# Kernel tuning notes

Hardware: AMD Instinct MI355X
Metric: run time of the kernel (lower is better)

The kernel has to match this reference:

```python
import jax, jax.numpy as jnp
import numpy as np

B = 256
D = 512
C = 100000
S = 30.0
M = 0.5
COS_M = float(np.cos(M))
SIN_M = float(np.sin(M))
TH = float(np.cos(np.pi - M))
MM = float(np.sin(np.pi - M) * M)


def setup_inputs() -> dict:
    key = jax.random.key(0)
    k1, k2, k3, k4 = jax.random.split(key, 4)
    image_emb = jax.random.normal(k1, (B, D), dtype=jnp.float32)
    profile_emb = jax.random.normal(k2, (B, D), dtype=jnp.float32)
    # xavier_uniform_ for weight [C, D]: bound = sqrt(6/(C+D))
    bound = float(np.sqrt(6.0 / (C + D)))
    weight = jax.random.uniform(k3, (C, D), dtype=jnp.float32, minval=-bound, maxval=bound)
    label = jax.random.randint(k4, (B,), 0, C, dtype=jnp.int64)
    return {"image_emb": image_emb, "profile_emb": profile_emb, "weight": weight, "label": label}


def reference(image_emb, profile_emb, weight, label):
    emb = jnp.concatenate([image_emb, profile_emb], axis=0)          # [2B, D]
    lab = jnp.tile(label, (2,))                                      # [2B]
    emb_n = emb / jnp.linalg.norm(emb, axis=1, keepdims=True)
    w_n = weight / jnp.linalg.norm(weight, axis=1, keepdims=True)
    cosine = jnp.einsum('nd,cd->nc', emb_n, w_n)                     # [2B, C]
    sine = jnp.sqrt(jnp.clip(1.0 - cosine * cosine, 0.0, 1.0))
    phi = cosine * COS_M - sine * SIN_M
    phi = jnp.where(cosine > TH, phi, cosine - MM)                   # easy_margin=False
    one_hot = jnp.arange(cosine.shape[1])[None, :] == lab[:, None]   # [2B, C] bool
    logits = S * jnp.where(one_hot, phi, cosine)
    logp = jax.nn.log_softmax(logits, axis=1)
    nll = -jnp.take_along_axis(logp, lab[:, None], axis=1)[:, 0]
    return jnp.mean(nll)
```

## Files before the change

kernel.cpp:

```cpp
#include <hip/hip_runtime.h>

#define S_SCALE 30.0f
#define COS_M 0.8775825618903728f
#define SIN_M 0.479425538604203f
#define TH_C (-0.8775825618903728f)
#define MM_C 0.2397127693021015f

#define BD 512
#define DD 512
#define CC 100000
#define NCB 1563
#define LASTB 1562

typedef __bf16 bf16x8 __attribute__((ext_vector_type(8)));
typedef __bf16 bf16x4 __attribute__((ext_vector_type(4)));
typedef float  f32x4  __attribute__((ext_vector_type(4)));

__global__ __launch_bounds__(256) void k_prep(const float* __restrict__ img,
                                              const float* __restrict__ prof,
                                              const float* __restrict__ W,
                                              const int* __restrict__ lab,
                                              __bf16* __restrict__ At,
                                              float* __restrict__ sphi,
                                              float* __restrict__ scos) {
    const int t = threadIdx.x;
    const int wave = t >> 6, l = t & 63;
    const int row = blockIdx.x * 4 + wave;
    const float* src = (row < 256) ? (img + (size_t)row * DD) : (prof + (size_t)(row - 256) * DD);
    float4 v0 = ((const float4*)src)[l * 2];
    float4 v1 = ((const float4*)src)[l * 2 + 1];
    float s = v0.x * v0.x + v0.y * v0.y + v0.z * v0.z + v0.w * v0.w
            + v1.x * v1.x + v1.y * v1.y + v1.z * v1.z + v1.w * v1.w;
    #pragma unroll
    for (int o = 1; o < 64; o <<= 1) s += __shfl_xor(s, o);
    float r = rsqrtf(s);
    bf16x8 a;
    a[0] = (__bf16)(v0.x * r); a[1] = (__bf16)(v0.y * r);
    a[2] = (__bf16)(v0.z * r); a[3] = (__bf16)(v0.w * r);
    a[4] = (__bf16)(v1.x * r); a[5] = (__bf16)(v1.y * r);
    a[6] = (__bf16)(v1.z * r); a[7] = (__bf16)(v1.w * r);
    *(bf16x8*)(At + (size_t)(l >> 2) * (BD * 32) + row * 32 + (l & 3) * 8) = a;

    const int c = lab[row & 255];
    const float4* wc = (const float4*)(W + (size_t)c * DD);
    float4 w0 = wc[l * 2], w1 = wc[l * 2 + 1];
    float wb0 = (float)(__bf16)w0.x, wb1 = (float)(__bf16)w0.y;
    float wb2 = (float)(__bf16)w0.z, wb3 = (float)(__bf16)w0.w;
    float wb4 = (float)(__bf16)w1.x, wb5 = (float)(__bf16)w1.y;
    float wb6 = (float)(__bf16)w1.z, wb7 = (float)(__bf16)w1.w;
    float dot = (float)a[0] * wb0 + (float)a[1] * wb1 + (float)a[2] * wb2 + (float)a[3] * wb3
              + (float)a[4] * wb4 + (float)a[5] * wb5 + (float)a[6] * wb6 + (float)a[7] * wb7;
    float wsq = wb0 * wb0 + wb1 * wb1 + wb2 * wb2 + wb3 * wb3
              + wb4 * wb4 + wb5 * wb5 + wb6 * wb6 + wb7 * wb7;
    #pragma unroll
    for (int o = 1; o < 64; o <<= 1) { dot += __shfl_xor(dot, o); wsq += __shfl_xor(wsq, o); }
    if (l == 0) {
        float cs = dot * rsqrtf(wsq);
        float sn = sqrtf(fmaxf(0.f, fminf(1.f, 1.f - cs * cs)));
        float phi = cs * COS_M - sn * SIN_M;
        if (!(cs > TH_C)) phi = cs - MM_C;
        sphi[row] = S_SCALE * phi;
        scos[row] = S_SCALE * cs;
    }
}

__global__ __launch_bounds__(256, 2) void k_gemm(const __bf16* __restrict__ At,
                                                 const float* __restrict__ W,
                                                 float* __restrict__ part) {
    __shared__ __bf16 Bs[2][64 * 32];
    __shared__ float  csq[64];

    const int t = threadIdx.x;
    const int cb = blockIdx.x;
    const int wave = t >> 6, lane = t & 63, q = lane >> 4, m16 = lane & 15;

    const int frag_off = m16 * 32 + ((q ^ ((m16 >> 1) & 3)) << 3);

    const int wcol = t >> 3, kc = t & 7;
    int gc0 = cb * 64 + wcol;
    int gc1 = gc0 + 32;
    const float* wp0 = W + (size_t)(gc0 < CC ? gc0 : 0) * DD + kc * 4;
    const float* wp1 = W + (size_t)(gc1 < CC ? gc1 : 0) * DD + kc * 4;
    const int sxw   = (kc >> 1) ^ ((wcol >> 1) & 3);
    const int wofs0 = wcol * 32 + sxw * 8 + (kc & 1) * 4;
    const int wofs1 = wofs0 + 1024;

    const __bf16* ap = At + (size_t)(wave * 128 + m16) * 32 + q * 8;

    f32x4 acc[8][4] = {};
    float sq0 = 0.f, sq1 = 0.f;
    bf16x8 a[2][8];
    float4 wv0[16], wv1[16];

#define CVT_BS(buf, va, vb)                                                             \
    {                                                                                   \
        bf16x4 b0 = { (__bf16)(va).x, (__bf16)(va).y, (__bf16)(va).z, (__bf16)(va).w }; \
        bf16x4 b1 = { (__bf16)(vb).x, (__bf16)(vb).y, (__bf16)(vb).z, (__bf16)(vb).w }; \
        float f;                                                                        \
        f = (float)b0[0]; sq0 += f * f; f = (float)b0[1]; sq0 += f * f;                 \
        f = (float)b0[2]; sq0 += f * f; f = (float)b0[3]; sq0 += f * f;                 \
        f = (float)b1[0]; sq1 += f * f; f = (float)b1[1]; sq1 += f * f;                 \
        f = (float)b1[2]; sq1 += f * f; f = (float)b1[3]; sq1 += f * f;                 \
        *(bf16x4*)(&Bs[buf][wofs0]) = b0;                                               \
        *(bf16x4*)(&Bs[buf][wofs1]) = b1;                                               \
    }

    #pragma unroll
    for (int i = 0; i < 8; ++i)
        a[0][i] = *(const bf16x8*)(ap + i * 512);
    wv0[0] = *(const float4*)(wp0);        wv1[0] = *(const float4*)(wp1);
    wv0[1] = *(const float4*)(wp0 + 32);   wv1[1] = *(const float4*)(wp1 + 32);
    wv0[2] = *(const float4*)(wp0 + 64);   wv1[2] = *(const float4*)(wp1 + 64);
    CVT_BS(0, wv0[0], wv1[0]);

    #pragma unroll
    for (int kt = 0; kt < 16; ++kt) {
        if (kt < 15) {
            #pragma unroll
            for (int i = 0; i < 8; ++i)
                a[(kt + 1) & 1][i] = *(const bf16x8*)(ap + (kt + 1) * 16384 + i * 512);
        }
        if (kt + 3 < 16) {
            wv0[kt + 3] = *(const float4*)(wp0 + (kt + 3) * 32);
            wv1[kt + 3] = *(const float4*)(wp1 + (kt + 3) * 32);
        }
        __builtin_amdgcn_sched_barrier(0);
        asm volatile("s_waitcnt lgkmcnt(0)");
        __builtin_amdgcn_s_barrier();
        __builtin_amdgcn_sched_barrier(0);

        bf16x8 bfrag[4];
        #pragma unroll
        for (int j = 0; j < 4; ++j)
            bfrag[j] = *(const bf16x8*)(&Bs[kt & 1][j * 512 + frag_off]);

        if (kt < 15) CVT_BS((kt + 1) & 1, wv0[kt + 1], wv1[kt + 1]);

        __builtin_amdgcn_s_setprio(1);
        #pragma unroll
        for (int i = 0; i < 8; ++i) {
            #pragma unroll
            for (int j = 0; j < 4; ++j)
                acc[i][j] = __builtin_amdgcn_mfma_f32_16x16x32_bf16(a[kt & 1][i], bfrag[j],
                                                                    acc[i][j], 0, 0, 0);
        }
        __builtin_amdgcn_s_setprio(0);
    }

    sq0 += __shfl_xor(sq0, 1); sq1 += __shfl_xor(sq1, 1);
    sq0 += __shfl_xor(sq0, 2); sq1 += __shfl_xor(sq1, 2);
    sq0 += __shfl_xor(sq0, 4); sq1 += __shfl_xor(sq1, 4);
    if (kc == 0) { csq[wcol] = sq0; csq[wcol + 32] = sq1; }
    __syncthreads();

    const bool lastb = (cb == LASTB);
    float inv[4]; bool val[4];
    #pragma unroll
    for (int j = 0; j < 4; ++j) {
        int ct = j * 16 + m16;
        val[j] = (!lastb) || (ct < 32);
        inv[j] = rsqrtf(csq[ct]) * S_SCALE;
    }
    #pragma unroll
    for (int i = 0; i < 8; ++i) {
        #pragma unroll
        for (int r = 0; r < 4; ++r) {
            float e = 0.f;
            #pragma unroll
            for (int j = 0; j < 4; ++j)
                if (val[j]) e += __expf(acc[i][j][r] * inv[j]);
            e += __shfl_xor(e, 1);
            e += __shfl_xor(e, 2);
            e += __shfl_xor(e, 4);
            e += __shfl_xor(e, 8);
            if (m16 == 0)
                part[(size_t)cb * BD + wave * 128 + i * 16 + q * 4 + r] = e;
        }
    }
#undef CVT_BS
}

__global__ __launch_bounds__(256) void k_reduce1(const float* __restrict__ part,
                                                 float* __restrict__ rowpart) {
    const int b = blockIdx.x;
    const int rg = b >> 5, cp = b & 31;
    const int t = threadIdx.x;
    const int rl = t & 63, ph = t >> 6;
    const int r0 = rg * 64;
    float s = 0.f;
    for (int c0 = cp * 4 + ph; c0 < NCB; c0 += 128)
        s += part[(size_t)c0 * BD + r0 + rl];
    __shared__ float buf[256];
    buf[t] = s;
    __syncthreads();
    if (t < 64)
        rowpart[(size_t)cp * BD + r0 + t] = buf[t] + buf[t + 64] + buf[t + 128] + buf[t + 192];
}

__global__ __launch_bounds__(256) void k_final(const float* __restrict__ rowpart,
                                               const float* __restrict__ sphi,
                                               const float* __restrict__ scos,
                                               float* __restrict__ out) {
    const int t = threadIdx.x;
    float a = 0.f;
    for (int r = t; r < BD; r += 256) {
        float total = 0.f;
        #pragma unroll
        for (int cp = 0; cp < 32; ++cp)
            total += rowpart[(size_t)cp * BD + r];
        float lse = logf(total);
        float sp = sphi[r], sc = scos[r];
        float corr = log1pf(__expf(sp - lse) - __expf(sc - lse));
        a += lse + corr - sp;
    }
    for (int o = 1; o < 64; o <<= 1) a += __shfl_xor(a, o);
    __shared__ float wsum[4];
    if ((t & 63) == 0) wsum[t >> 6] = a;
    __syncthreads();
    if (t == 0) out[0] = (wsum[0] + wsum[1] + wsum[2] + wsum[3]) * (1.0f / 512.0f);
}

extern "C" void kernel_launch(void* const* d_in, const int* in_sizes, int n_in,
                              void* d_out, int out_size, void* d_ws, size_t ws_size,
                              hipStream_t stream) {
    const float* img  = (const float*)d_in[0];
    const float* prof = (const float*)d_in[1];
    const float* W    = (const float*)d_in[2];
    const int*   lab  = (const int*)d_in[3];

    char* ws = (char*)d_ws;
    __bf16* At     = (__bf16*)ws;
    float* sphi    = (float*)(ws + 524288);
    float* scos    = (float*)(ws + 526336);
    float* part    = (float*)(ws + 528384);
    float* rowpart = (float*)(ws + 3729408);

    k_prep<<<128, 256, 0, stream>>>(img, prof, W, lab, At, sphi, scos);
    k_gemm<<<NCB, 256, 0, stream>>>(At, W, part);
    k_reduce1<<<256, 256, 0, stream>>>(part, rowpart);
    k_final<<<1, 256, 0, stream>>>(rowpart, sphi, scos, (float*)d_out);
}
```

Before: 325.9 us.

## Ring-buffer A fragments and interleave next-tile loads with split MFMA halves

Replaces the double-buffered 16-entry A fragment array with a 12-slot ring. The next tile's A loads are split into two halves, each issued around one half of the MFMA block, so fewer vector registers stay live. The W prefetch becomes a 4-deep rotating buffer, up from 3-ahead. The bf16 conversion and LDS store of the next W tile now happen after the MFMAs. The aim is to lower register pressure and overlap global loads with matrix math. The risk is exposing load latency inside the MFMA sequence and delaying the LDS write before the next barrier.

```diff
diff --git a/kernel.cpp b/kernel.cpp
--- a/kernel.cpp
+++ b/kernel.cpp
@@ -89,8 +89,8 @@
 
     f32x4 acc[8][4] = {};
     float sq0 = 0.f, sq1 = 0.f;
-    bf16x8 a[2][8];
-    float4 wv0[16], wv1[16];
+    bf16x8 ar[12];
+    float4 wva[4], wvb[4];
 
 #define CVT_BS(buf, va, vb)                                                             \
     {                                                                                   \
@@ -106,24 +106,28 @@
     }
 
     #pragma unroll
-    for (int i = 0; i < 8; ++i)
-        a[0][i] = *(const bf16x8*)(ap + i * 512);
-    wv0[0] = *(const float4*)(wp0);        wv1[0] = *(const float4*)(wp1);
-    wv0[1] = *(const float4*)(wp0 + 32);   wv1[1] = *(const float4*)(wp1 + 32);
-    wv0[2] = *(const float4*)(wp0 + 64);   wv1[2] = *(const float4*)(wp1 + 64);
-    CVT_BS(0, wv0[0], wv1[0]);
+    for (int f = 0; f < 8; ++f)
+        ar[f] = *(const bf16x8*)(ap + f * 512);
+    #pragma unroll
+    for (int n = 0; n < 4; ++n) {
+        wva[n] = *(const float4*)(wp0 + n * 32);
+        wvb[n] = *(const float4*)(wp1 + n * 32);
+    }
+    CVT_BS(0, wva[0], wvb[0]);
 
     #pragma unroll
     for (int kt = 0; kt < 16; ++kt) {
+        if (kt + 4 < 16) {
+            wva[(kt + 4) & 3] = *(const float4*)(wp0 + (kt + 4) * 32);
+            wvb[(kt + 4) & 3] = *(const float4*)(wp1 + (kt + 4) * 32);
+        }
         if (kt < 15) {
             #pragma unroll
-            for (int i = 0; i < 8; ++i)
-                a[(kt + 1) & 1][i] = *(const bf16x8*)(ap + (kt + 1) * 16384 + i * 512);
-        }
-        if (kt + 3 < 16) {
-            wv0[kt + 3] = *(const float4*)(wp0 + (kt + 3) * 32);
-            wv1[kt + 3] = *(const float4*)(wp1 + (kt + 3) * 32);
-        }
+            for (int f = 0; f < 4; ++f)
+                ar[((kt + 1) * 8 + f) % 12] =
+                    *(const bf16x8*)(ap + (kt + 1) * 16384 + f * 512);
+        }
+
         __builtin_amdgcn_sched_barrier(0);
         asm volatile("s_waitcnt lgkmcnt(0)");
         __builtin_amdgcn_s_barrier();
@@ -134,17 +138,35 @@
         for (int j = 0; j < 4; ++j)
             bfrag[j] = *(const bf16x8*)(&Bs[kt & 1][j * 512 + frag_off]);
 
-        if (kt < 15) CVT_BS((kt + 1) & 1, wv0[kt + 1], wv1[kt + 1]);
-
         __builtin_amdgcn_s_setprio(1);
         #pragma unroll
-        for (int i = 0; i < 8; ++i) {
+        for (int i = 0; i < 4; ++i) {
             #pragma unroll
             for (int j = 0; j < 4; ++j)
-                acc[i][j] = __builtin_amdgcn_mfma_f32_16x16x32_bf16(a[kt & 1][i], bfrag[j],
-                                                                    acc[i][j], 0, 0, 0);
+                acc[i][j] = __builtin_amdgcn_mfma_f32_16x16x32_bf16(
+                    ar[(kt * 8 + i) % 12], bfrag[j], acc[i][j], 0, 0, 0);
         }
         __builtin_amdgcn_s_setprio(0);
+
+        if (kt < 15) {
+            #pragma unroll
+            for (int f = 4; f < 8; ++f)
+                ar[((kt + 1) * 8 + f) % 12] =
+                    *(const bf16x8*)(ap + (kt + 1) * 16384 + f * 512);
+        }
+
+        __builtin_amdgcn_s_setprio(1);
+        #pragma unroll
+        for (int i = 4; i < 8; ++i) {
+            #pragma unroll
+            for (int j = 0; j < 4; ++j)
+                acc[i][j] = __builtin_amdgcn_mfma_f32_16x16x32_bf16(
+                    ar[(kt * 8 + i) % 12], bfrag[j], acc[i][j], 0, 0, 0);
+        }
+        __builtin_amdgcn_s_setprio(0);
+
+        __builtin_amdgcn_sched_barrier(0);
+        if (kt < 15) CVT_BS((kt + 1) & 1, wva[(kt + 1) & 3], wvb[(kt + 1) & 3]);
     }
 
     sq0 += __shfl_xor(sq0, 1); sq1 += __shfl_xor(sq1, 1);
```

New measurement: 325.6 us. No clear change (-0.1%).

## Widen GEMM tile to 128 classes and stage activations via direct global-to-LDS loads

Applied to the files above, without the earlier changes.

Each GEMM block now uses 512 threads and covers 128 weight columns instead of 64, arranged as 2 column groups by 4 row groups of waves. The bf16 activation tile is streamed into shared memory with global_load_lds across a 4-deep ring, so waves share it instead of each loading A fragments into registers. Weight loads are pipelined four tiles ahead with hand-tuned vmcnt waits, and the partial-sum layout and reduction bounds are updated to match. This aims to halve redundant activation traffic per class and free registers. In exchange it uses much more LDS (about 144KB per block), which may limit occupancy, and the hand-counted waits are fragile.

```diff
diff --git a/kernel.cpp b/kernel.cpp
--- a/kernel.cpp
+++ b/kernel.cpp
@@ -9,12 +9,15 @@
 #define BD 512
 #define DD 512
 #define CC 100000
-#define NCB 1563
-#define LASTB 1562
+#define NCB2 782
+#define LASTB2 781
+#define NPART 1564
 
 typedef __bf16 bf16x8 __attribute__((ext_vector_type(8)));
-typedef __bf16 bf16x4 __attribute__((ext_vector_type(4)));
 typedef float  f32x4  __attribute__((ext_vector_type(4)));
+
+#define AS1 __attribute__((address_space(1)))
+#define AS3 __attribute__((address_space(3)))
 
 __global__ __launch_bounds__(256) void k_prep(const float* __restrict__ img,
                                               const float* __restrict__ prof,
@@ -64,100 +67,120 @@
     }
 }
 
-__global__ __launch_bounds__(256, 2) void k_gemm(const __bf16* __restrict__ At,
+__global__ __launch_bounds__(512, 2) void k_gemm(const __bf16* __restrict__ At,
                                                  const float* __restrict__ W,
                                                  float* __restrict__ part) {
-    __shared__ __bf16 Bs[2][64 * 32];
-    __shared__ float  csq[64];
+    __shared__ __bf16 As[4][BD * 32];
+    __shared__ __bf16 Bs[2][128 * 32];
+    __shared__ float  csq[128];
 
     const int t = threadIdx.x;
     const int cb = blockIdx.x;
     const int wave = t >> 6, lane = t & 63, q = lane >> 4, m16 = lane & 15;
+    const int rg = wave >> 1;
+    const int cg = wave & 1;
 
     const int frag_off = m16 * 32 + ((q ^ ((m16 >> 1) & 3)) << 3);
 
-    const int wcol = t >> 3, kc = t & 7;
-    int gc0 = cb * 64 + wcol;
-    int gc1 = gc0 + 32;
-    const float* wp0 = W + (size_t)(gc0 < CC ? gc0 : 0) * DD + kc * 4;
-    const float* wp1 = W + (size_t)(gc1 < CC ? gc1 : 0) * DD + kc * 4;
-    const int sxw   = (kc >> 1) ^ ((wcol >> 1) & 3);
-    const int wofs0 = wcol * 32 + sxw * 8 + (kc & 1) * 4;
-    const int wofs1 = wofs0 + 1024;
-
-    const __bf16* ap = At + (size_t)(wave * 128 + m16) * 32 + q * 8;
+    const int wcol = t >> 2, kc = t & 3;
+    const int gc = cb * 128 + wcol;
+    const float* wp = W + (size_t)(gc < CC ? gc : 0) * DD + kc * 8;
+    const int wofs = wcol * 32 + ((kc ^ ((wcol >> 1) & 3)) << 3);
+
+    const int srcswz = ((t >> 2) << 6) + ((((t & 3) ^ ((t >> 3) & 3))) << 4);
 
     f32x4 acc[8][4] = {};
-    float sq0 = 0.f, sq1 = 0.f;
-    bf16x8 a[2][8];
-    float4 wv0[16], wv1[16];
+    float sq = 0.f;
+    float4 wva[4], wvb[4];
+
+#define GLDS_TILE(kt, buf)                                                              \
+    {                                                                                   \
+        const char* gsrc = (const char*)At + (size_t)(kt) * 32768 + srcswz;             \
+        _Pragma("unroll")                                                               \
+        for (int c4 = 0; c4 < 4; ++c4) {                                                \
+            __builtin_amdgcn_global_load_lds(                                           \
+                (AS1 void*)(gsrc + c4 * 8192),                                          \
+                (AS3 void*)((char*)(&As[buf][0]) + c4 * 8192 + wave * 1024),            \
+                16, 0, 0);                                                              \
+        }                                                                               \
+    }
+
+#define LOAD_W(n)                                                                       \
+    {                                                                                   \
+        wva[(n) & 3] = *(const float4*)(wp + (n) * 32);                                 \
+        wvb[(n) & 3] = *(const float4*)(wp + (n) * 32 + 4);                             \
+    }
 
 #define CVT_BS(buf, va, vb)                                                             \
     {                                                                                   \
-        bf16x4 b0 = { (__bf16)(va).x, (__bf16)(va).y, (__bf16)(va).z, (__bf16)(va).w }; \
-        bf16x4 b1 = { (__bf16)(vb).x, (__bf16)(vb).y, (__bf16)(vb).z, (__bf16)(vb).w }; \
+        bf16x8 b;                                                                       \
+        b[0] = (__bf16)(va).x; b[1] = (__bf16)(va).y;                                   \
+        b[2] = (__bf16)(va).z; b[3] = (__bf16)(va).w;                                   \
+        b[4] = (__bf16)(vb).x; b[5] = (__bf16)(vb).y;                                   \
+        b[6] = (__bf16)(vb).z; b[7] = (__bf16)(vb).w;                                   \
         float f;                                                                        \
-        f = (float)b0[0]; sq0 += f * f; f = (float)b0[1]; sq0 += f * f;                 \
-        f = (float)b0[2]; sq0 += f * f; f = (float)b0[3]; sq0 += f * f;                 \
-        f = (float)b1[0]; sq1 += f * f; f = (float)b1[1]; sq1 += f * f;                 \
-        f = (float)b1[2]; sq1 += f * f; f = (float)b1[3]; sq1 += f * f;                 \
-        *(bf16x4*)(&Bs[buf][wofs0]) = b0;                                               \
-        *(bf16x4*)(&Bs[buf][wofs1]) = b1;                                               \
-    }
-
-    #pragma unroll
-    for (int i = 0; i < 8; ++i)
-        a[0][i] = *(const bf16x8*)(ap + i * 512);
-    wv0[0] = *(const float4*)(wp0);        wv1[0] = *(const float4*)(wp1);
-    wv0[1] = *(const float4*)(wp0 + 32);   wv1[1] = *(const float4*)(wp1 + 32);
-    wv0[2] = *(const float4*)(wp0 + 64);   wv1[2] = *(const float4*)(wp1 + 64);
-    CVT_BS(0, wv0[0], wv1[0]);
-
-    #pragma unroll
-    for (int kt = 0; kt < 16; ++kt) {
-        if (kt < 15) {
-            #pragma unroll
-            for (int i = 0; i < 8; ++i)
-                a[(kt + 1) & 1][i] = *(const bf16x8*)(ap + (kt + 1) * 16384 + i * 512);
-        }
-        if (kt + 3 < 16) {
-            wv0[kt + 3] = *(const float4*)(wp0 + (kt + 3) * 32);
-            wv1[kt + 3] = *(const float4*)(wp1 + (kt + 3) * 32);
-        }
-        __builtin_amdgcn_sched_barrier(0);
-        asm volatile("s_waitcnt lgkmcnt(0)");
-        __builtin_amdgcn_s_barrier();
-        __builtin_amdgcn_sched_barrier(0);
-
-        bf16x8 bfrag[4];
-        #pragma unroll
-        for (int j = 0; j < 4; ++j)
-            bfrag[j] = *(const bf16x8*)(&Bs[kt & 1][j * 512 + frag_off]);
-
-        if (kt < 15) CVT_BS((kt + 1) & 1, wv0[kt + 1], wv1[kt + 1]);
-
-        __builtin_amdgcn_s_setprio(1);
-        #pragma unroll
-        for (int i = 0; i < 8; ++i) {
-            #pragma unroll
-            for (int j = 0; j < 4; ++j)
-                acc[i][j] = __builtin_amdgcn_mfma_f32_16x16x32_bf16(a[kt & 1][i], bfrag[j],
-                                                                    acc[i][j], 0, 0, 0);
-        }
-        __builtin_amdgcn_s_setprio(0);
-    }
-
-    sq0 += __shfl_xor(sq0, 1); sq1 += __shfl_xor(sq1, 1);
-    sq0 += __shfl_xor(sq0, 2); sq1 += __shfl_xor(sq1, 2);
-    sq0 += __shfl_xor(sq0, 4); sq1 += __shfl_xor(sq1, 4);
-    if (kc == 0) { csq[wcol] = sq0; csq[wcol + 32] = sq1; }
+        f = (float)b[0]; sq += f * f; f = (float)b[1]; sq += f * f;                     \
+        f = (float)b[2]; sq += f * f; f = (float)b[3]; sq += f * f;                     \
+        f = (float)b[4]; sq += f * f; f = (float)b[5]; sq += f * f;                     \
+        f = (float)b[6]; sq += f * f; f = (float)b[7]; sq += f * f;                     \
+        *(bf16x8*)(&Bs[buf][wofs]) = b;                                                 \
+    }
+
+#define SB() __builtin_amdgcn_sched_barrier(0)
+
+#define ITER(kt, VM)                                                                    \
+    {                                                                                   \
+        if ((kt) + 2 <= 15) GLDS_TILE((kt) + 2, ((kt) + 2) & 3);                        \
+        SB();                                                                           \
+        if ((kt) + 4 <= 15) LOAD_W((kt) + 4);                                           \
+        SB();                                                                           \
+        asm volatile("s_waitcnt vmcnt(" #VM ") lgkmcnt(0)" ::: "memory");               \
+        __builtin_amdgcn_s_barrier();                                                   \
+        SB();                                                                           \
+        bf16x8 bfrag[4];                                                                \
+        _Pragma("unroll")                                                               \
+        for (int j = 0; j < 4; ++j)                                                     \
+            bfrag[j] = *(const bf16x8*)(&Bs[(kt) & 1][cg * 2048 + j * 512 + frag_off]); \
+        __builtin_amdgcn_s_setprio(1);                                                  \
+        _Pragma("unroll")                                                               \
+        for (int i = 0; i < 8; ++i) {                                                   \
+            bf16x8 afrag =                                                              \
+                *(const bf16x8*)(&As[(kt) & 3][rg * 4096 + i * 512 + frag_off]);        \
+            _Pragma("unroll")                                                           \
+            for (int j = 0; j < 4; ++j)                                                 \
+                acc[i][j] = __builtin_amdgcn_mfma_f32_16x16x32_bf16(                    \
+                    afrag, bfrag[j], acc[i][j], 0, 0, 0);                               \
+        }                                                                               \
+        __builtin_amdgcn_s_setprio(0);                                                  \
+        SB();                                                                           \
+        if ((kt) + 1 <= 15) CVT_BS(((kt) + 1) & 1, wva[((kt) + 1) & 3],                 \
+                                   wvb[((kt) + 1) & 3]);                                \
+    }
+
+    LOAD_W(0); LOAD_W(1);
+    SB();
+    GLDS_TILE(0, 0); GLDS_TILE(1, 1);
+    SB();
+    LOAD_W(2); LOAD_W(3);
+    SB();
+    CVT_BS(0, wva[0], wvb[0]);
+
+    ITER(0, 14);  ITER(1, 16);
+    ITER(2, 14);  ITER(3, 14);  ITER(4, 14);  ITER(5, 14);
+    ITER(6, 14);  ITER(7, 14);  ITER(8, 14);  ITER(9, 14);
+    ITER(10, 14); ITER(11, 14);
+    ITER(12, 12); ITER(13, 10); ITER(14, 4);  ITER(15, 0);
+
+    sq += __shfl_xor(sq, 1);
+    sq += __shfl_xor(sq, 2);
+    if (kc == 0) csq[wcol] = sq;
     __syncthreads();
 
-    const bool lastb = (cb == LASTB);
+    const bool lastb = (cb == LASTB2);
     float inv[4]; bool val[4];
     #pragma unroll
     for (int j = 0; j < 4; ++j) {
-        int ct = j * 16 + m16;
+        int ct = cg * 64 + j * 16 + m16;
         val[j] = (!lastb) || (ct < 32);
         inv[j] = rsqrtf(csq[ct]) * S_SCALE;
     }
@@ -174,10 +197,14 @@
             e += __shfl_xor(e, 4);
             e += __shfl_xor(e, 8);
             if (m16 == 0)
-                part[(size_t)cb * BD + wave * 128 + i * 16 + q * 4 + r] = e;
+                part[((size_t)cb * 2 + cg) * BD + rg * 128 + i * 16 + q * 4 + r] = e;
         }
     }
+#undef GLDS_TILE
+#undef LOAD_W
 #undef CVT_BS
+#undef SB
+#undef ITER
 }
 
 __global__ __launch_bounds__(256) void k_reduce1(const float* __restrict__ part,
@@ -188,7 +215,7 @@
     const int rl = t & 63, ph = t >> 6;
     const int r0 = rg * 64;
     float s = 0.f;
-    for (int c0 = cp * 4 + ph; c0 < NCB; c0 += 128)
+    for (int c0 = cp * 4 + ph; c0 < NPART; c0 += 128)
         s += part[(size_t)c0 * BD + r0 + rl];
     __shared__ float buf[256];
     buf[t] = s;
@@ -233,10 +260,10 @@
     float* sphi    = (float*)(ws + 524288);
     float* scos    = (float*)(ws + 526336);
     float* part    = (float*)(ws + 528384);
-    float* rowpart = (float*)(ws + 3729408);
+    float* rowpart = (float*)(ws + 3731456);
 
     k_prep<<<128, 256, 0, stream>>>(img, prof, W, lab, At, sphi, scos);
-    k_gemm<<<NCB, 256, 0, stream>>>(At, W, part);
+    k_gemm<<<NCB2, 512, 0, stream>>>(At, W, part);
     k_reduce1<<<256, 256, 0, stream>>>(part, rowpart);
     k_final<<<1, 256, 0, stream>>>(rowpart, sphi, scos, (float*)d_out);
 }
```

Result: slower. 344.9 us (+5.8%).

## Retile GEMM to 128x128 blocks with LDS-staged A via global_load_lds

Applied to the files above, without the earlier changes.

The GEMM is restructured from 64-class blocks holding all 512 rows in registers to 128-row by 128-class tiles with a 2x2 wave layout. A tiles are streamed into LDS via direct global-to-LDS loads instead of per-wave register loads. A block-index swizzle groups the four row blocks of a class tile, and occupancy is raised to 3 blocks per CU through a smaller accumulator footprint. Each W tile is now read and converted four times, once per row block, which raises W traffic unless L2 absorbs the repeats. The last block's validity mask (ct < 32) may be wrong for wc=1 under the new 128-class tiling.

```diff
diff --git a/kernel.cpp b/kernel.cpp
--- a/kernel.cpp
+++ b/kernel.cpp
@@ -9,12 +9,15 @@
 #define BD 512
 #define DD 512
 #define CC 100000
-#define NCB 1563
-#define LASTB 1562
+#define NCB2 782
+#define LASTB2 781
+#define NPART 1564
 
 typedef __bf16 bf16x8 __attribute__((ext_vector_type(8)));
-typedef __bf16 bf16x4 __attribute__((ext_vector_type(4)));
 typedef float  f32x4  __attribute__((ext_vector_type(4)));
+
+#define AS1 __attribute__((address_space(1)))
+#define AS3 __attribute__((address_space(3)))
 
 __global__ __launch_bounds__(256) void k_prep(const float* __restrict__ img,
                                               const float* __restrict__ prof,
@@ -64,105 +67,130 @@
     }
 }
 
-__global__ __launch_bounds__(256, 2) void k_gemm(const __bf16* __restrict__ At,
+__global__ __launch_bounds__(256, 3) void k_gemm(const __bf16* __restrict__ At,
                                                  const float* __restrict__ W,
                                                  float* __restrict__ part) {
-    __shared__ __bf16 Bs[2][64 * 32];
-    __shared__ float  csq[64];
-
-    const int t = threadIdx.x;
-    const int cb = blockIdx.x;
+    __shared__ __bf16 As[2][128 * 32];
+    __shared__ __bf16 Bs[2][128 * 32];
+
+    const int t = threadIdx.x;
+    const int bid = blockIdx.x;
+    const int swz = (bid & 7) * 391 + (bid >> 3);
+    const int rb = swz & 3;
+    const int cb = swz >> 2;
     const int wave = t >> 6, lane = t & 63, q = lane >> 4, m16 = lane & 15;
+    const int wr = wave >> 1, wc = wave & 1;
 
     const int frag_off = m16 * 32 + ((q ^ ((m16 >> 1) & 3)) << 3);
 
-    const int wcol = t >> 3, kc = t & 7;
-    int gc0 = cb * 64 + wcol;
-    int gc1 = gc0 + 32;
-    const float* wp0 = W + (size_t)(gc0 < CC ? gc0 : 0) * DD + kc * 4;
-    const float* wp1 = W + (size_t)(gc1 < CC ? gc1 : 0) * DD + kc * 4;
-    const int sxw   = (kc >> 1) ^ ((wcol >> 1) & 3);
-    const int wofs0 = wcol * 32 + sxw * 8 + (kc & 1) * 4;
-    const int wofs1 = wofs0 + 1024;
-
-    const __bf16* ap = At + (size_t)(wave * 128 + m16) * 32 + q * 8;
-
-    f32x4 acc[8][4] = {};
-    float sq0 = 0.f, sq1 = 0.f;
-    bf16x8 a[2][8];
-    float4 wv0[16], wv1[16];
-
-#define CVT_BS(buf, va, vb)                                                             \
-    {                                                                                   \
-        bf16x4 b0 = { (__bf16)(va).x, (__bf16)(va).y, (__bf16)(va).z, (__bf16)(va).w }; \
-        bf16x4 b1 = { (__bf16)(vb).x, (__bf16)(vb).y, (__bf16)(vb).z, (__bf16)(vb).w }; \
+    const int wcol = t >> 1, h = t & 1;
+    const int gc = cb * 128 + wcol;
+    const float* wp = W + (size_t)(gc < CC ? gc : 0) * DD + h * 16;
+    const int bofs0 = wcol * 32 + (((h * 2 + 0) ^ ((wcol >> 1) & 3)) << 3);
+    const int bofs1 = wcol * 32 + (((h * 2 + 1) ^ ((wcol >> 1) & 3)) << 3);
+
+    const int srcswz = ((t >> 2) << 6) + ((((t & 3) ^ ((t >> 3) & 3))) << 4);
+    const char* abase = (const char*)At + (size_t)rb * 8192 + srcswz;
+
+    f32x4 acc[4][4] = {};
+    float sq = 0.f;
+    float4 wr0, wr1, wr2, wr3;
+    bf16x8 nb0, nb1;
+
+#define GLDS_TILE(kt, buf)                                                              \
+    {                                                                                   \
+        _Pragma("unroll")                                                               \
+        for (int rr = 0; rr < 2; ++rr) {                                                \
+            __builtin_amdgcn_global_load_lds(                                           \
+                (AS1 void*)(abase + (size_t)(kt) * 32768 + rr * 4096),                  \
+                (AS3 void*)((char*)(&As[buf][0]) + rr * 4096 + wave * 1024),            \
+                16, 0, 0);                                                              \
+        }                                                                               \
+    }
+
+#define LOADW(n)                                                                        \
+    {                                                                                   \
+        wr0 = *(const float4*)(wp + (n) * 32);                                          \
+        wr1 = *(const float4*)(wp + (n) * 32 + 4);                                      \
+        wr2 = *(const float4*)(wp + (n) * 32 + 8);                                      \
+        wr3 = *(const float4*)(wp + (n) * 32 + 12);                                     \
+    }
+
+#define CVTW()                                                                          \
+    {                                                                                   \
+        nb0[0] = (__bf16)wr0.x; nb0[1] = (__bf16)wr0.y;                                 \
+        nb0[2] = (__bf16)wr0.z; nb0[3] = (__bf16)wr0.w;                                 \
+        nb0[4] = (__bf16)wr1.x; nb0[5] = (__bf16)wr1.y;                                 \
+        nb0[6] = (__bf16)wr1.z; nb0[7] = (__bf16)wr1.w;                                 \
+        nb1[0] = (__bf16)wr2.x; nb1[1] = (__bf16)wr2.y;                                 \
+        nb1[2] = (__bf16)wr2.z; nb1[3] = (__bf16)wr2.w;                                 \
+        nb1[4] = (__bf16)wr3.x; nb1[5] = (__bf16)wr3.y;                                 \
+        nb1[6] = (__bf16)wr3.z; nb1[7] = (__bf16)wr3.w;                                 \
         float f;                                                                        \
-        f = (float)b0[0]; sq0 += f * f; f = (float)b0[1]; sq0 += f * f;                 \
-        f = (float)b0[2]; sq0 += f * f; f = (float)b0[3]; sq0 += f * f;                 \
-        f = (float)b1[0]; sq1 += f * f; f = (float)b1[1]; sq1 += f * f;                 \
-        f = (float)b1[2]; sq1 += f * f; f = (float)b1[3]; sq1 += f * f;                 \
-        *(bf16x4*)(&Bs[buf][wofs0]) = b0;                                               \
-        *(bf16x4*)(&Bs[buf][wofs1]) = b1;                                               \
-    }
-
-    #pragma unroll
-    for (int i = 0; i < 8; ++i)
-        a[0][i] = *(const bf16x8*)(ap + i * 512);
-    wv0[0] = *(const float4*)(wp0);        wv1[0] = *(const float4*)(wp1);
-    wv0[1] = *(const float4*)(wp0 + 32);   wv1[1] = *(const float4*)(wp1 + 32);
-    wv0[2] = *(const float4*)(wp0 + 64);   wv1[2] = *(const float4*)(wp1 + 64);
-    CVT_BS(0, wv0[0], wv1[0]);
+        f = (float)nb0[0]; sq += f * f; f = (float)nb0[1]; sq += f * f;                 \
+        f = (float)nb0[2]; sq += f * f; f = (float)nb0[3]; sq += f * f;                 \
+        f = (float)nb0[4]; sq += f * f; f = (float)nb0[5]; sq += f * f;                 \
+        f = (float)nb0[6]; sq += f * f; f = (float)nb0[7]; sq += f * f;                 \
+        f = (float)nb1[0]; sq += f * f; f = (float)nb1[1]; sq += f * f;                 \
+        f = (float)nb1[2]; sq += f * f; f = (float)nb1[3]; sq += f * f;                 \
+        f = (float)nb1[4]; sq += f * f; f = (float)nb1[5]; sq += f * f;                 \
+        f = (float)nb1[6]; sq += f * f; f = (float)nb1[7]; sq += f * f;                 \
+    }
+
+#define WRITEBS(buf)                                                                    \
+    {                                                                                   \
+        *(bf16x8*)(&Bs[buf][bofs0]) = nb0;                                              \
+        *(bf16x8*)(&Bs[buf][bofs1]) = nb1;                                              \
+    }
+
+    GLDS_TILE(0, 0);
+    LOADW(0);
+    CVTW();
+    WRITEBS(0);
+    LOADW(1);
 
     #pragma unroll
     for (int kt = 0; kt < 16; ++kt) {
+        __syncthreads();
         if (kt < 15) {
-            #pragma unroll
-            for (int i = 0; i < 8; ++i)
-                a[(kt + 1) & 1][i] = *(const bf16x8*)(ap + (kt + 1) * 16384 + i * 512);
+            GLDS_TILE(kt + 1, (kt + 1) & 1);
+            CVTW();
+            WRITEBS((kt + 1) & 1);
         }
-        if (kt + 3 < 16) {
-            wv0[kt + 3] = *(const float4*)(wp0 + (kt + 3) * 32);
-            wv1[kt + 3] = *(const float4*)(wp1 + (kt + 3) * 32);
-        }
-        __builtin_amdgcn_sched_barrier(0);
-        asm volatile("s_waitcnt lgkmcnt(0)");
-        __builtin_amdgcn_s_barrier();
-        __builtin_amdgcn_sched_barrier(0);
-
-        bf16x8 bfrag[4];
+        if (kt < 14) LOADW(kt + 2);
+
+        bf16x8 bfrag[4], afrag[4];
         #pragma unroll
         for (int j = 0; j < 4; ++j)
-            bfrag[j] = *(const bf16x8*)(&Bs[kt & 1][j * 512 + frag_off]);
-
-        if (kt < 15) CVT_BS((kt + 1) & 1, wv0[kt + 1], wv1[kt + 1]);
-
-        __builtin_amdgcn_s_setprio(1);
-        #pragma unroll
-        for (int i = 0; i < 8; ++i) {
+            bfrag[j] = *(const bf16x8*)(&Bs[kt & 1][wc * 2048 + j * 512 + frag_off]);
+        #pragma unroll
+        for (int i = 0; i < 4; ++i)
+            afrag[i] = *(const bf16x8*)(&As[kt & 1][wr * 2048 + i * 512 + frag_off]);
+        #pragma unroll
+        for (int i = 0; i < 4; ++i) {
             #pragma unroll
             for (int j = 0; j < 4; ++j)
-                acc[i][j] = __builtin_amdgcn_mfma_f32_16x16x32_bf16(a[kt & 1][i], bfrag[j],
-                                                                    acc[i][j], 0, 0, 0);
+                acc[i][j] = __builtin_amdgcn_mfma_f32_16x16x32_bf16(
+                    afrag[i], bfrag[j], acc[i][j], 0, 0, 0);
         }
-        __builtin_amdgcn_s_setprio(0);
-    }
-
-    sq0 += __shfl_xor(sq0, 1); sq1 += __shfl_xor(sq1, 1);
-    sq0 += __shfl_xor(sq0, 2); sq1 += __shfl_xor(sq1, 2);
-    sq0 += __shfl_xor(sq0, 4); sq1 += __shfl_xor(sq1, 4);
-    if (kc == 0) { csq[wcol] = sq0; csq[wcol + 32] = sq1; }
-    __syncthreads();
-
-    const bool lastb = (cb == LASTB);
+    }
+
+    __syncthreads();
+    float* csq = (float*)&As[0][0];
+    sq += __shfl_xor(sq, 1);
+    if (h == 0) csq[wcol] = sq;
+    __syncthreads();
+
+    const bool lastb = (cb == LASTB2);
     float inv[4]; bool val[4];
     #pragma unroll
     for (int j = 0; j < 4; ++j) {
-        int ct = j * 16 + m16;
+        int ct = wc * 64 + j * 16 + m16;
         val[j] = (!lastb) || (ct < 32);
         inv[j] = rsqrtf(csq[ct]) * S_SCALE;
     }
     #pragma unroll
-    for (int i = 0; i < 8; ++i) {
+    for (int i = 0; i < 4; ++i) {
         #pragma unroll
         for (int r = 0; r < 4; ++r) {
             float e = 0.f;
@@ -174,10 +202,13 @@
             e += __shfl_xor(e, 4);
             e += __shfl_xor(e, 8);
             if (m16 == 0)
-                part[(size_t)cb * BD + wave * 128 + i * 16 + q * 4 + r] = e;
+                part[((size_t)cb * 2 + wc) * BD + rb * 128 + wr * 64 + i * 16 + q * 4 + r] = e;
         }
     }
-#undef CVT_BS
+#undef GLDS_TILE
+#undef LOADW
+#undef CVTW
+#undef WRITEBS
 }
 
 __global__ __launch_bounds__(256) void k_reduce1(const float* __restrict__ part,
@@ -188,7 +219,7 @@
     const int rl = t & 63, ph = t >> 6;
     const int r0 = rg * 64;
     float s = 0.f;
-    for (int c0 = cp * 4 + ph; c0 < NCB; c0 += 128)
+    for (int c0 = cp * 4 + ph; c0 < NPART; c0 += 128)
         s += part[(size_t)c0 * BD + r0 + rl];
     __shared__ float buf[256];
     buf[t] = s;
@@ -233,10 +264,10 @@
     float* sphi    = (float*)(ws + 524288);
     float* scos    = (float*)(ws + 526336);
     float* part    = (float*)(ws + 528384);
-    float* rowpart = (float*)(ws + 3729408);
+    float* rowpart = (float*)(ws + 3731456);
 
     k_prep<<<128, 256, 0, stream>>>(img, prof, W, lab, At, sphi, scos);
-    k_gemm<<<NCB, 256, 0, stream>>>(At, W, part);
+    k_gemm<<<4 * NCB2, 256, 0, stream>>>(At, W, part);
     k_reduce1<<<256, 256, 0, stream>>>(part, rowpart);
     k_final<<<1, 256, 0, stream>>>(rowpart, sphi, scos, (float*)d_out);
 }
```

New measurement: 357.2 us. 1.1x slower.
